# Kernel tuning notes

Measured on AMD Instinct MI355X. Metric: run time of the kernel, lower is better.

The kernel has to match this reference:

```python
import jax, jax.numpy as jnp
import numpy as np

B, T, K, H = 4, 2048, 1024, 16
D = K // H

def setup_inputs() -> dict:
    key = jax.random.key(0)
    kx, kq, kk, kv = jax.random.split(key, 4)
    s = 1.0 / np.sqrt(K)
    return {
        "x": jax.random.normal(kx, (B, T, K), dtype=jnp.float32),
        "Wq": jax.random.normal(kq, (K, K), dtype=jnp.float32) * s,
        "Wk": jax.random.normal(kk, (K, K), dtype=jnp.float32) * s,
        "Wv": jax.random.normal(kv, (K, K), dtype=jnp.float32) * s,
    }

def reference(x, Wq, Wk, Wv):
    b, t, k = x.shape
    h, d = H, K // H
    # projections -> (b, h, t, d)
    q = (x @ Wq.T).reshape(b, t, h, d).transpose(0, 2, 1, 3)
    ke = (x @ Wk.T).reshape(b, t, h, d).transpose(0, 2, 1, 3)
    v = (x @ Wv.T).reshape(b, t, h, d).transpose(0, 2, 1, 3)
    scale = d ** (-0.25)  # applied to both q and k, as in the original
    scores = jnp.einsum('bhqd,bhkd->bhqk', q * scale, ke * scale)
    causal = jnp.triu(jnp.ones((t, t), dtype=bool), k=1)
    scores = jnp.where(causal, -jnp.inf, scores)
    attn = jax.nn.softmax(scores, axis=-1)
    out = jnp.einsum('bhqk,bhkd->bhqd', attn, v)
    return out.transpose(0, 2, 1, 3).reshape(b, t, k)
```

## Files before the change

### kernel.cpp

```cpp
#include <hip/hip_runtime.h>
#include <hip/hip_bf16.h>
#include <math.h>

#define B_   4
#define T_   2048
#define KDIM 1024
#define H_   16
#define D_   64
#define BH_  (B_*H_)
#define M_   (B_*T_)
#define NKT  (KDIM/64)

typedef __bf16 bf16;
typedef __bf16 bf16x8 __attribute__((ext_vector_type(8)));
typedef __bf16 bf16x4 __attribute__((ext_vector_type(4)));
typedef float  f32x4  __attribute__((ext_vector_type(4)));
typedef float  f32x16 __attribute__((ext_vector_type(16)));
typedef unsigned int u32;
typedef u32 u32x4 __attribute__((ext_vector_type(4)));

static __device__ __forceinline__ f32x4 mfma16(bf16x8 a, bf16x8 b, f32x4 c) {
    return __builtin_amdgcn_mfma_f32_16x16x32_bf16(a, b, c, 0, 0, 0);
}
static __device__ __forceinline__ f32x16 mfma32(bf16x8 a, bf16x8 b, f32x16 c) {
    return __builtin_amdgcn_mfma_f32_32x32x16_bf16(a, b, c, 0, 0, 0);
}
static __device__ __forceinline__ float exp2_fast(float x) {
    float r; asm("v_exp_f32 %0, %1" : "=v"(r) : "v"(x)); return r;
}

__global__ void cvt_all(const float* __restrict__ x,  const float* __restrict__ Wq,
                        const float* __restrict__ Wk, const float* __restrict__ Wv,
                        bf16* __restrict__ dst) {
    int i = blockIdx.x * blockDim.x + threadIdx.x;
    const int NX = M_*KDIM/4, NW = KDIM*KDIM/4;
    const float* src;
    int j;
    if (i < NX)                { src = x;  j = i; }
    else if (i < NX + NW)      { src = Wq; j = i - NX; }
    else if (i < NX + 2*NW)    { src = Wk; j = i - NX - NW; }
    else                       { src = Wv; j = i - NX - 2*NW; }
    float4 v = reinterpret_cast<const float4*>(src)[j];
    bf16x4 o;
    o.x = (bf16)v.x; o.y = (bf16)v.y; o.z = (bf16)v.z; o.w = (bf16)v.w;
    reinterpret_cast<bf16x4*>(dst)[i] = o;
}

__global__ __launch_bounds__(256) void proj_gemm97(
    const bf16* __restrict__ xb, const bf16* __restrict__ Wflat,
    bf16* __restrict__ Qb, bf16* __restrict__ Kb, bf16* __restrict__ Vtb)
{
    __shared__ __align__(16) char Asm[128*128];
    __shared__ __align__(16) char Bsm[128*128];

    const int tid  = threadIdx.x;
    const int wid  = tid >> 6;
    const int lane = tid & 63;
    const int l15  = lane & 15, l4 = lane >> 4;
    const int wr = wid >> 1, wc = wid & 1;

    const int orig = blockIdx.x;
    const int xcd  = orig & 7;
    const int idx  = orig >> 3;
    const int mblk = xcd * 8 + (idx & 7);
    const int nblk = idx >> 3;
    const int row0 = mblk * 128, col0 = nblk * 128;

    const bf16* aS[4]; const bf16* bS[4];
#pragma unroll
    for (int q = 0; q < 4; ++q) {
        int c   = q*256 + tid;
        int rr  = c >> 3;
        int cb  = (c & 7) * 16;
        int cbs = cb ^ ((rr & 7) << 4);
        aS[q] = xb    + (size_t)(row0 + rr)*KDIM + (cbs >> 1);
        bS[q] = Wflat + (size_t)(col0 + rr)*KDIM + (cbs >> 1);
    }

    f32x4 acc[4][4] = {};
    const int sw   = (l15 & 7) << 4;
    const int arow = (wr*64 + l15) * 128;
    const int brow = (wc*64 + l15) * 128;

    for (int kt = 0; kt < NKT; ++kt) {
        const int k0 = kt * 64;
        __syncthreads();
#pragma unroll
        for (int q = 0; q < 4; ++q) {
            char* la = Asm + (q*256 + wid*64)*16;
            __builtin_amdgcn_global_load_lds(
                (const __attribute__((address_space(1))) void*)(aS[q] + k0),
                (__attribute__((address_space(3))) void*)la, 16, 0, 0);
        }
#pragma unroll
        for (int q = 0; q < 4; ++q) {
            char* lb = Bsm + (q*256 + wid*64)*16;
            __builtin_amdgcn_global_load_lds(
                (const __attribute__((address_space(1))) void*)(bS[q] + k0),
                (__attribute__((address_space(3))) void*)lb, 16, 0, 0);
        }
        asm volatile("s_waitcnt vmcnt(0)" ::: "memory");
        __syncthreads();

#pragma unroll
        for (int kk = 0; kk < 2; ++kk) {
            const int cbk = (kk*64 + l4*16) ^ sw;
            bf16x8 af[4], bfr[4];
#pragma unroll
            for (int m = 0; m < 4; ++m)
                af[m] = *reinterpret_cast<const bf16x8*>(Asm + arow + m*2048 + cbk);
#pragma unroll
            for (int n = 0; n < 4; ++n)
                bfr[n] = *reinterpret_cast<const bf16x8*>(Bsm + brow + n*2048 + cbk);
#pragma unroll
            for (int m = 0; m < 4; ++m)
#pragma unroll
                for (int n = 0; n < 4; ++n)
                    acc[m][n] = mfma16(af[m], bfr[n], acc[m][n]);
        }
    }

#pragma unroll
    for (int m = 0; m < 4; ++m)
#pragma unroll
        for (int n = 0; n < 4; ++n)
#pragma unroll
            for (int r = 0; r < 4; ++r) {
                int gi = row0 + wr*64 + m*16 + l4*4 + r;
                int gj = col0 + wc*64 + n*16 + l15;
                int wz  = gj >> 10;
                int gjw = gj & 1023;
                float v = acc[m][n][r];
                if (wz == 0) v *= 0.18033688011112042f;
                bf16 o = (bf16)v;
                int bb = gi >> 11, tt = gi & (T_-1);
                int hh = gjw >> 6, dd = gjw & (D_-1);
                size_t bh = (size_t)bb*H_ + hh;
                if (wz == 0)      Qb [(bh*T_ + tt)*D_ + dd] = o;
                else if (wz == 1) Kb [(bh*T_ + tt)*D_ + dd] = o;
                else              Vtb[(bh*D_ + dd)*T_ + tt] = o;
            }
}

__global__ __launch_bounds__(256) void flash_attn3(
    const bf16* __restrict__ Qb, const bf16* __restrict__ Kb,
    const bf16* __restrict__ Vtb, float* __restrict__ out)
{
    __shared__ __align__(16) char Ksm[8192];
    __shared__ __align__(16) char Vsm[8192];

    const int tid  = threadIdx.x;
    const int wid  = tid >> 6;
    const int lane = tid & 63;
    const int l31  = lane & 31;
    const int hi   = lane >> 5;

    const int orig = blockIdx.x;
    const int wg   = (orig & 7) * 128 + (orig >> 3);
    const int bh   = wg >> 4;
    const int qblk = (15 - (wg & 15)) * 128;
    const int q0   = qblk + wid * 32;
    const int q_abs = q0 + l31;

    const bf16* qp = Qb + ((size_t)bh*T_ + q_abs)*D_ + hi*8;
    bf16x8 qf[4];
#pragma unroll
    for (int j = 0; j < 4; ++j)
        qf[j] = *reinterpret_cast<const bf16x8*>(qp + j*16);

    const bf16* kbase = Kb  + (size_t)bh*T_*D_;
    const bf16* vbase = Vtb + (size_t)bh*D_*T_;

    f32x16 o0 = {}; f32x16 o1 = {};
    float lsum = 0.f;

    const int my_nt  = (q0 + 31) >> 6;
    const int blk_nt = qblk/64 + 1;
    const int tmaskb = q_abs - 4*hi;

    const int r0 = tid >> 3,          r1 = (tid + 256) >> 3;
    const int e0 = (tid & 7) * 8;
    const u32 lds0 = (u32)((r0*128 + e0*2) ^ ((r0 & 7) << 4));
    const u32 lds1 = (u32)((r1*128 + e0*2) ^ ((r1 & 7) << 4));

    u32x4 kr0, kr1, vr0, vr1;
    auto issue = [&](int nt) {
        kr0 = *reinterpret_cast<const u32x4*>(kbase + ((size_t)(nt*64 + r0))*D_ + e0);
        kr1 = *reinterpret_cast<const u32x4*>(kbase + ((size_t)(nt*64 + r1))*D_ + e0);
        vr0 = *reinterpret_cast<const u32x4*>(vbase + (size_t)r0*T_ + nt*64 + e0);
        vr1 = *reinterpret_cast<const u32x4*>(vbase + (size_t)r1*T_ + nt*64 + e0);
    };
    issue(0);

    auto subtile = [&](int s, int kvb_abs, bool maskit, bf16x8& pA, bf16x8& pB) {
        f32x16 sacc = {};
        const int row = s*32 + l31;
        const int swk = (row & 7) << 4;
#pragma unroll
        for (int j = 0; j < 4; ++j) {
            bf16x8 kf = *reinterpret_cast<const bf16x8*>(Ksm + ((row*128 + j*32 + hi*16) ^ swk));
            sacc = mfma32(kf, qf[j], sacc);
        }
        const int tlim = tmaskb - kvb_abs;
        float p[16];
#pragma unroll
        for (int r = 0; r < 16; ++r) {
            const int crow0 = (r & 3) + 8*(r >> 2);
            float sv = sacc[r];
            if (maskit) sv = (crow0 > tlim) ? -INFINITY : sv;
            p[r] = exp2_fast(sv);
        }
        {
            float a0 = p[0]+p[1],   a1 = p[2]+p[3],   a2 = p[4]+p[5],   a3 = p[6]+p[7];
            float a4 = p[8]+p[9],   a5 = p[10]+p[11], a6 = p[12]+p[13], a7 = p[14]+p[15];
            lsum += ((a0+a1) + (a2+a3)) + ((a4+a5) + (a6+a7));
        }
        u32 w[8];
#pragma unroll
        for (int i = 0; i < 8; ++i) {
            u32 wv;
            asm("v_cvt_pk_bf16_f32 %0, %1, %2" : "=v"(wv) : "v"(p[2*i]), "v"(p[2*i+1]));
            w[i] = wv;
        }
        u32 a0w = w[0], a2w = w[2];
        asm("v_permlane32_swap_b32 %0, %1" : "+v"(a0w), "+v"(a2w));
        u32 a1w = w[1], a3w = w[3];
        asm("v_permlane32_swap_b32 %0, %1" : "+v"(a1w), "+v"(a3w));
        u32 b0w = w[4], b2w = w[6];
        asm("v_permlane32_swap_b32 %0, %1" : "+v"(b0w), "+v"(b2w));
        u32 b1w = w[5], b3w = w[7];
        asm("v_permlane32_swap_b32 %0, %1" : "+v"(b1w), "+v"(b3w));
        u32x4 A0 = {a0w, a1w, a2w, a3w};
        u32x4 A1 = {b0w, b1w, b2w, b3w};
        pA = __builtin_bit_cast(bf16x8, A0);
        pB = __builtin_bit_cast(bf16x8, A1);
    };

    auto pv = [&](int ks, bf16x8 pf) {
        const int swv = (l31 & 7) << 4;
        const int colb = ks*32 + hi*16;
        bf16x8 v0 = *reinterpret_cast<const bf16x8*>(Vsm + ((l31*128 + colb) ^ swv));
        bf16x8 v1 = *reinterpret_cast<const bf16x8*>(Vsm + (((32 + l31)*128 + colb) ^ swv));
        o0 = mfma32(v0, pf, o0);
        o1 = mfma32(v1, pf, o1);
    };

    for (int nt = 0; nt <= blk_nt; ++nt) {
        __syncthreads();
        *reinterpret_cast<u32x4*>(Ksm + lds0) = kr0;
        *reinterpret_cast<u32x4*>(Ksm + lds1) = kr1;
        *reinterpret_cast<u32x4*>(Vsm + lds0) = vr0;
        *reinterpret_cast<u32x4*>(Vsm + lds1) = vr1;
        __syncthreads();
        if (nt < blk_nt) issue(nt + 1);

        if (nt <= my_nt) {
            const bool partial = (nt == my_nt);
            const int  nsub = (!partial || (q0 & 32)) ? 2 : 1;
            bf16x8 pA, pB;
            subtile(0, nt*64, partial, pA, pB);
            pv(0, pA);
            pv(1, pB);
            if (nsub == 2) {
                subtile(1, nt*64 + 32, partial, pA, pB);
                pv(2, pA);
                pv(3, pB);
            }
        }
    }

    lsum += __shfl_xor(lsum, 32);
    const float inv = 1.0f / lsum;
    const int bb = bh >> 4, hh = bh & 15;
    float* orow = out + ((size_t)bb*T_ + q_abs)*KDIM + hh*64 + hi*4;
#pragma unroll
    for (int g = 0; g < 4; ++g) {
        f32x4 v0, v1;
#pragma unroll
        for (int j = 0; j < 4; ++j) { v0[j] = o0[g*4+j]*inv; v1[j] = o1[g*4+j]*inv; }
        *reinterpret_cast<f32x4*>(orow + g*8)      = v0;
        *reinterpret_cast<f32x4*>(orow + 32 + g*8) = v1;
    }
}

extern "C" void kernel_launch(void* const* d_in, const int* in_sizes, int n_in,
                              void* d_out, int out_size, void* d_ws, size_t ws_size,
                              hipStream_t stream) {
    (void)in_sizes; (void)n_in; (void)out_size; (void)ws_size;
    const float* x  = (const float*)d_in[0];
    const float* Wq = (const float*)d_in[1];
    const float* Wk = (const float*)d_in[2];
    const float* Wv = (const float*)d_in[3];
    float* out = (float*)d_out;

    bf16* xb  = (bf16*)d_ws;
    bf16* Wb  = xb + (size_t)M_*KDIM;
    bf16* Qb  = Wb + (size_t)3*KDIM*KDIM;
    bf16* Kb  = Qb + (size_t)M_*KDIM;
    bf16* Vtb = Kb + (size_t)M_*KDIM;

    const int n4 = (M_*KDIM + 3*KDIM*KDIM) / 4;
    cvt_all<<<(n4 + 255)/256, 256, 0, stream>>>(x, Wq, Wk, Wv, xb);

    proj_gemm97<<<dim3(1536), 256, 0, stream>>>(xb, Wb, Qb, Kb, Vtb);
    flash_attn3<<<dim3(BH_*16), 256, 0, stream>>>(Qb, Kb, Vtb, out);
}
```

Measured before the change: 163.1 us.

## Double-buffer LDS tiles in projection GEMM to overlap loads with MFMA

Converts the projection GEMM from a single LDS buffer into two ping-pong buffers. Tile t+2 is prefetched via global_load_lds while tile t is computed, and partial vmcnt waits let the next tile's loads stay in flight. MFMA blocks are also wrapped in s_setprio to favour compute issue. This doubles LDS use to 64KB per block, which may reduce occupancy, and adds an extra barrier per iteration.

```diff
diff --git a/kernel.cpp b/kernel.cpp
--- a/kernel.cpp
+++ b/kernel.cpp
@@ -46,12 +46,12 @@
     reinterpret_cast<bf16x4*>(dst)[i] = o;
 }
 
-__global__ __launch_bounds__(256) void proj_gemm97(
+__global__ __launch_bounds__(256) void proj_gemm_db(
     const bf16* __restrict__ xb, const bf16* __restrict__ Wflat,
     bf16* __restrict__ Qb, bf16* __restrict__ Kb, bf16* __restrict__ Vtb)
 {
-    __shared__ __align__(16) char Asm[128*128];
-    __shared__ __align__(16) char Bsm[128*128];
+    __shared__ __align__(16) char As[2][16384];
+    __shared__ __align__(16) char Bs[2][16384];
 
     const int tid  = threadIdx.x;
     const int wid  = tid >> 6;
@@ -77,46 +77,71 @@
         bS[q] = Wflat + (size_t)(col0 + rr)*KDIM + (cbs >> 1);
     }
 
+    auto stage = [&](int kt, int buf) {
+        if (kt >= NKT) return;
+        const int k0 = kt * 64;
+#pragma unroll
+        for (int q = 0; q < 4; ++q) {
+            char* la = As[buf] + (q*256 + wid*64)*16;
+            __builtin_amdgcn_global_load_lds(
+                (const __attribute__((address_space(1))) void*)(aS[q] + k0),
+                (__attribute__((address_space(3))) void*)la, 16, 0, 0);
+        }
+#pragma unroll
+        for (int q = 0; q < 4; ++q) {
+            char* lb = Bs[buf] + (q*256 + wid*64)*16;
+            __builtin_amdgcn_global_load_lds(
+                (const __attribute__((address_space(1))) void*)(bS[q] + k0),
+                (__attribute__((address_space(3))) void*)lb, 16, 0, 0);
+        }
+    };
+
     f32x4 acc[4][4] = {};
     const int sw   = (l15 & 7) << 4;
     const int arow = (wr*64 + l15) * 128;
     const int brow = (wc*64 + l15) * 128;
 
-    for (int kt = 0; kt < NKT; ++kt) {
-        const int k0 = kt * 64;
-        __syncthreads();
-#pragma unroll
-        for (int q = 0; q < 4; ++q) {
-            char* la = Asm + (q*256 + wid*64)*16;
-            __builtin_amdgcn_global_load_lds(
-                (const __attribute__((address_space(1))) void*)(aS[q] + k0),
-                (__attribute__((address_space(3))) void*)la, 16, 0, 0);
-        }
-#pragma unroll
-        for (int q = 0; q < 4; ++q) {
-            char* lb = Bsm + (q*256 + wid*64)*16;
-            __builtin_amdgcn_global_load_lds(
-                (const __attribute__((address_space(1))) void*)(bS[q] + k0),
-                (__attribute__((address_space(3))) void*)lb, 16, 0, 0);
-        }
-        asm volatile("s_waitcnt vmcnt(0)" ::: "memory");
-        __syncthreads();
-
+    stage(0, 0);
+    stage(1, 1);
+
+    for (int t = 0; t < NKT; ++t) {
+        const int bt = t & 1;
+        if (t + 1 < NKT) {
+            asm volatile("s_waitcnt vmcnt(8)" ::: "memory");
+        } else {
+            asm volatile("s_waitcnt vmcnt(0)" ::: "memory");
+        }
+        __builtin_amdgcn_sched_barrier(0);
+        __builtin_amdgcn_s_barrier();
+        __builtin_amdgcn_sched_barrier(0);
+
+        const char* Ap = As[bt];
+        const char* Bp = Bs[bt];
 #pragma unroll
         for (int kk = 0; kk < 2; ++kk) {
             const int cbk = (kk*64 + l4*16) ^ sw;
             bf16x8 af[4], bfr[4];
 #pragma unroll
             for (int m = 0; m < 4; ++m)
-                af[m] = *reinterpret_cast<const bf16x8*>(Asm + arow + m*2048 + cbk);
+                af[m] = *reinterpret_cast<const bf16x8*>(Ap + arow + m*2048 + cbk);
 #pragma unroll
             for (int n = 0; n < 4; ++n)
-                bfr[n] = *reinterpret_cast<const bf16x8*>(Bsm + brow + n*2048 + cbk);
+                bfr[n] = *reinterpret_cast<const bf16x8*>(Bp + brow + n*2048 + cbk);
+            __builtin_amdgcn_s_setprio(1);
 #pragma unroll
             for (int m = 0; m < 4; ++m)
 #pragma unroll
                 for (int n = 0; n < 4; ++n)
                     acc[m][n] = mfma16(af[m], bfr[n], acc[m][n]);
+            __builtin_amdgcn_s_setprio(0);
+        }
+
+        if (t + 2 < NKT) {
+            asm volatile("s_waitcnt lgkmcnt(0)" ::: "memory");
+            __builtin_amdgcn_sched_barrier(0);
+            __builtin_amdgcn_s_barrier();
+            __builtin_amdgcn_sched_barrier(0);
+            stage(t + 2, bt);
         }
     }
 
@@ -302,6 +327,6 @@
     const int n4 = (M_*KDIM + 3*KDIM*KDIM) / 4;
     cvt_all<<<(n4 + 255)/256, 256, 0, stream>>>(x, Wq, Wk, Wv, xb);
 
-    proj_gemm97<<<dim3(1536), 256, 0, stream>>>(xb, Wb, Qb, Kb, Vtb);
+    proj_gemm_db<<<dim3(1536), 256, 0, stream>>>(xb, Wb, Qb, Kb, Vtb);
     flash_attn3<<<dim3(BH_*16), 256, 0, stream>>>(Qb, Kb, Vtb, out);
 }
```

Result: faster. 155.1 us (-4.9%).
